# Kernel optimization log

Measured on AMD Instinct MI355X. Metric: run time of the kernel, lower is better.

## Reference

```python
import jax, jax.numpy as jnp
import numpy as np

BETA = 0.99  # EMA momentum from init_kwargs
EPS = 1e-12  # torch F.normalize eps


def _normalize(v):
    # matches torch.nn.functional.normalize (L2, dim=-1, eps clamp)
    n = jnp.maximum(jnp.linalg.norm(v, axis=-1, keepdims=True), EPS)
    return v / n


def setup_inputs() -> dict:
    key = jax.random.key(0)
    k1, k2 = jax.random.split(key)
    x = jax.random.normal(k1, (16384, 1024), dtype=jnp.float32)
    group_features = jax.random.uniform(k2, (8192, 1024), dtype=jnp.float32)
    return {"x": x, "group_features": group_features}


def reference(x, group_features):
    n_groups = group_features.shape[0]
    # assign_groups: cosine-sim argmax (normalized copies; does NOT modify x used below)
    xn = _normalize(x)
    gn = _normalize(group_features)
    logits = xn @ gn.T                      # [B, G]
    assignments = jnp.argmax(logits, axis=-1)  # [B] int

    # bincount over groups
    counts = jax.ops.segment_sum(
        jnp.ones_like(assignments, dtype=jnp.int32), assignments, num_segments=n_groups
    )  # [G]

    # scale only groups that received at least one sample by beta
    gf = jnp.where((counts > 0)[:, None], group_features * BETA, group_features)

    # scatter-add EMA contribution: (1-beta) * mean-style sum of raw x per group
    per_sample = x / counts[assignments][:, None].astype(x.dtype)  # safe: count>=1 for assigned
    contrib = jax.ops.segment_sum(per_sample, assignments, num_segments=n_groups)  # [G, D]
    gf = gf + (1.0 - BETA) * contrib

    return _normalize(gf)
```

## Files before the change

### kernel.cpp

```cpp
#include <hip/hip_runtime.h>

#define B_N 16384
#define G_N 8192
#define D_N 1024
#define NT 96

typedef unsigned short u16;
typedef unsigned long long u64;
typedef __attribute__((ext_vector_type(8))) short short8;
typedef __attribute__((ext_vector_type(16))) float f32x16;

#define AS1 __attribute__((address_space(1)))
#define AS3 __attribute__((address_space(3)))


__global__ __launch_bounds__(256) void k_norms(const float* __restrict__ g,
                                               float* __restrict__ invn) {
    const int j = blockIdx.x;
    const int t = threadIdx.x;
    const float4 v = *reinterpret_cast<const float4*>(&g[(size_t)j * D_N + t * 4]);
    float s = v.x * v.x + v.y * v.y + v.z * v.z + v.w * v.w;
#pragma unroll
    for (int off = 32; off >= 1; off >>= 1) s += __shfl_down(s, off, 64);
    __shared__ float wsum[4];
    if ((t & 63) == 0) wsum[t >> 6] = s;
    __syncthreads();
    if (t == 0) {
        const float tot = wsum[0] + wsum[1] + wsum[2] + wsum[3];
        invn[j] = 1.0f / fmaxf(sqrtf(tot), 1e-12f);
    }
}

__global__ void k_counts(const u64* __restrict__ pk, int* __restrict__ counts) {
    const int i = blockIdx.x * blockDim.x + threadIdx.x;
    if (i < B_N) {
        const int a = 8191 - (int)(pk[i] & 0x1FFFull);
        atomicAdd(&counts[a], 1);
    }
}

__global__ __launch_bounds__(256) void k_scatter(const float* __restrict__ x,
                                                 const u64* __restrict__ pk,
                                                 const int* __restrict__ counts,
                                                 float* __restrict__ contrib) {
    const int i = blockIdx.x;
    const int a = 8191 - (int)(pk[i] & 0x1FFFull);
    const float scale = 1.0f / (float)counts[a];
    const int t = threadIdx.x;
    const float4 v = *reinterpret_cast<const float4*>(&x[(size_t)i * D_N + t * 4]);
    float* dst = &contrib[(size_t)a * D_N + t * 4];
    atomicAdd(dst + 0, v.x * scale);
    atomicAdd(dst + 1, v.y * scale);
    atomicAdd(dst + 2, v.z * scale);
    atomicAdd(dst + 3, v.w * scale);
}

__global__ __launch_bounds__(256) void k_finalize(const float* __restrict__ g,
                                                  const int* __restrict__ counts,
                                                  float* __restrict__ out) {
    const int j = blockIdx.x;
    const int t = threadIdx.x;
    const float sc = (counts[j] > 0) ? 0.99f : 1.0f;
    const float4 gv = *reinterpret_cast<const float4*>(&g[(size_t)j * D_N + t * 4]);
    const float4 cv = *reinterpret_cast<const float4*>(&out[(size_t)j * D_N + t * 4]);
    float4 gf;
    gf.x = sc * gv.x + 0.01f * cv.x;
    gf.y = sc * gv.y + 0.01f * cv.y;
    gf.z = sc * gv.z + 0.01f * cv.z;
    gf.w = sc * gv.w + 0.01f * cv.w;
    float s = gf.x * gf.x + gf.y * gf.y + gf.z * gf.z + gf.w * gf.w;
#pragma unroll
    for (int off = 32; off >= 1; off >>= 1) s += __shfl_down(s, off, 64);
    __shared__ float wsum[4];
    __shared__ float s_inv;
    if ((t & 63) == 0) wsum[t >> 6] = s;
    __syncthreads();
    if (t == 0) s_inv = 1.0f / fmaxf(sqrtf(wsum[0] + wsum[1] + wsum[2] + wsum[3]), 1e-12f);
    __syncthreads();
    gf.x *= s_inv; gf.y *= s_inv; gf.z *= s_inv; gf.w *= s_inv;
    *reinterpret_cast<float4*>(&out[(size_t)j * D_N + t * 4]) = gf;
}


__device__ inline u16 f2bf_rtn(float f) {
    unsigned u = __float_as_uint(f);
    unsigned r = u + 0x7fffu + ((u >> 16) & 1u);
    return (u16)(r >> 16);
}
__device__ inline float bf2f(u16 h) { return __uint_as_float(((unsigned)h) << 16); }

__global__ __launch_bounds__(256) void k_split_pack(const float* __restrict__ src,
                                                    u16* __restrict__ hi,
                                                    u16* __restrict__ lo) {
    const int id = blockIdx.x * 256 + threadIdx.x;
    const int brick = id >> 7, c = id & 127;
    const int mu = brick >> 5, tau = brick & 31;
    const int ks = c >> 6, lane = c & 63;
    const int row = mu * 32 + (lane & 31);
    const int k = tau * 32 + ks * 16 + (lane >> 5) * 8;
    const float* s = src + (size_t)row * D_N + k;
    const float4 v0 = *reinterpret_cast<const float4*>(s);
    const float4 v1 = *reinterpret_cast<const float4*>(s + 4);
    const float f[8] = {v0.x, v0.y, v0.z, v0.w, v1.x, v1.y, v1.z, v1.w};
    short8 h, l;
#pragma unroll
    for (int j = 0; j < 8; ++j) {
        const u16 hj = f2bf_rtn(f[j]);
        h[j] = (short)hj;
        l[j] = (short)f2bf_rtn(f[j] - bf2f(hj));
    }
    *reinterpret_cast<short8*>(hi + (size_t)id * 8) = h;
    *reinterpret_cast<short8*>(lo + (size_t)id * 8) = l;
}


#define MFMA_BLK(S) do {                                                                   \
    __builtin_amdgcn_s_setprio(1);                                                         \
    _Pragma("unroll")                                                                      \
    for (int m = 0; m < 4; ++m)                                                            \
        _Pragma("unroll")                                                                  \
        for (int ks = 0; ks < 2; ++ks)                                                     \
            _Pragma("unroll")                                                              \
            for (int n = 0; n < 4; ++n)                                                    \
                acc[m][n] = __builtin_amdgcn_mfma_f32_32x32x16_bf16(                       \
                    afr[S][m][ks], bfr[S][n][ks], acc[m][n], 0, 0, 0);                     \
    __builtin_amdgcn_s_setprio(0);                                                         \
} while (0)

#define READS(BUF, S) do {                                                                 \
    const u16* aB = lds + (BUF) * 16384 + aRd;                                             \
    const u16* bB = lds + (BUF) * 16384 + 8192 + bRd;                                      \
    _Pragma("unroll")                                                                      \
    for (int n = 0; n < 4; ++n)                                                            \
        _Pragma("unroll")                                                                  \
        for (int ks = 0; ks < 2; ++ks)                                                     \
            bfr[S][n][ks] = *reinterpret_cast<const short8*>(bB + n * 1024 + ks * 512);    \
    _Pragma("unroll")                                                                      \
    for (int m = 0; m < 4; ++m)                                                            \
        _Pragma("unroll")                                                                  \
        for (int ks = 0; ks < 2; ++ks)                                                     \
            afr[S][m][ks] = *reinterpret_cast<const short8*>(aB + m * 1024 + ks * 512);    \
} while (0)

#define BODY(P, BRD, BSTG, SM, SR) do {                                                    \
    READS(BRD, SR);                                                                        \
    STG((P) + 3, BSTG);                                                                    \
    __builtin_amdgcn_sched_barrier(0);                                                     \
    MFMA_BLK(SM);                                                                          \
    asm volatile("s_waitcnt vmcnt(8)" ::: "memory");                                       \
    __builtin_amdgcn_s_barrier();                                                          \
} while (0)

__global__ __launch_bounds__(256, 1) void k_gemm_argmax(
    const u16* __restrict__ x_hi, const u16* __restrict__ x_lo,
    const u16* __restrict__ g_hi, const u16* __restrict__ g_lo,
    const float* __restrict__ invn, u64* __restrict__ pk) {

    __shared__ __align__(16) u16 lds[65536];

    const int bid = blockIdx.x;
    const int xcd = bid & 7, lcl = bid >> 3;
    const int mblk = xcd * 8 + ((lcl >> 3) & 7);
    const int nblk = (lcl & 7) + (lcl >> 6) * 8;
    const int mrow0 = mblk * 256, nrow0 = nblk * 256;

    const int tid = threadIdx.x;
    const int lane = tid & 63;
    const int w = tid >> 6;
    const int wr = w >> 1, wc = w & 1;
    const int l31 = lane & 31, l5 = lane >> 5;

    const int aRd = wr * 4096 + lane * 8;
    const int bRd = wc * 4096 + lane * 8;

    const int cOff = (tid & 127) * 8;
    const int hb = tid >> 7;
    const int wub = (tid & 192) * 8;
    const size_t aBase = ((size_t)(mblk * 8 + hb)) * 32768 + cOff;
    const size_t bBase = ((size_t)(nblk * 8 + hb)) * 32768 + cOff;

    auto STG = [&](int T, int buf) {
        const int Tc = T < NT ? T : NT - 1;
        const int term = Tc >> 5;
        const int tko = (Tc & 31) * 1024;
        const u16* xa = ((term == 1) ? x_lo : x_hi) + aBase + tko;
        const u16* gb = ((term == 2) ? g_lo : g_hi) + bBase + tko;
        u16* da = lds + buf * 16384 + wub;
        u16* db = da + 8192;
#pragma unroll
        for (int i = 0; i < 4; ++i)
            __builtin_amdgcn_global_load_lds((const AS1 void*)(xa + (size_t)i * 65536),
                                             (AS3 void*)(da + i * 2048), 16, 0, 0);
#pragma unroll
        for (int i = 0; i < 4; ++i)
            __builtin_amdgcn_global_load_lds((const AS1 void*)(gb + (size_t)i * 65536),
                                             (AS3 void*)(db + i * 2048), 16, 0, 0);
    };

    f32x16 acc[4][4];
#pragma unroll
    for (int m = 0; m < 4; ++m)
#pragma unroll
        for (int n = 0; n < 4; ++n)
#pragma unroll
            for (int r = 0; r < 16; ++r) acc[m][n][r] = 0.0f;

    short8 afr[2][4][2], bfr[2][4][2];

    STG(0, 0); STG(1, 1); STG(2, 2);
    asm volatile("s_waitcnt vmcnt(8)" ::: "memory");
    __builtin_amdgcn_s_barrier();
    READS(0, 0);

    for (int it = 0; it < 24; ++it) {
        const int p = it * 4;
        BODY(p,     1, 3, 0, 1);
        BODY(p + 1, 2, 0, 1, 0);
        BODY(p + 2, 3, 1, 0, 1);
        BODY(p + 3, 0, 2, 1, 0);
    }

    float inv[4];
#pragma unroll
    for (int n = 0; n < 4; ++n) inv[n] = invn[nrow0 + wc * 128 + n * 32 + l31];

#pragma unroll
    for (int m = 0; m < 4; ++m) {
#pragma unroll
        for (int r = 0; r < 16; ++r) {
            u64 p = 0;
#pragma unroll
            for (int n = 0; n < 4; ++n) {
                const float v = acc[m][n][r] * inv[n];
                unsigned u = __float_as_uint(v);
                u ^= (u >> 31) ? 0xFFFFFFFFu : 0x80000000u;
                const int col = nrow0 + wc * 128 + n * 32 + l31;
                const u64 cand = ((u64)u << 13) | (unsigned)(8191 - col);
                p = (cand > p) ? cand : p;
            }
#pragma unroll
            for (int msk = 1; msk < 32; msk <<= 1) {
                const u64 o = __shfl_xor(p, msk, 64);
                p = (o > p) ? o : p;
            }
            if (l31 == 0) {
                const int row = mrow0 + wr * 128 + m * 32 + (r & 3) + 8 * (r >> 2) + 4 * l5;
                atomicMax(&pk[row], p);
            }
        }
    }
}


__global__ __launch_bounds__(256) void k_argmax_fp32(const float* __restrict__ x,
                                                     const float* __restrict__ g,
                                                     const float* __restrict__ invn,
                                                     int* __restrict__ assign) {
    __shared__ __align__(16) float As[32][68];
    __shared__ __align__(16) float Bs[32][68];
    const int t = threadIdx.x;
    const int tx = t & 15;
    const int ty = t >> 4;
    const int row0 = blockIdx.x * 64;
    const int r_a = t >> 3;
    const int c4 = t & 7;
    float bestv[4]; int besti[4];
#pragma unroll
    for (int i = 0; i < 4; ++i) { bestv[i] = -3.0e38f; besti[i] = 0; }
    for (int jt = 0; jt < G_N / 64; ++jt) {
        float acc[4][4] = {};
        for (int kt = 0; kt < D_N / 32; ++kt) {
#pragma unroll
            for (int p = 0; p < 2; ++p) {
                const int r = r_a + p * 32;
                const float4 va = *reinterpret_cast<const float4*>(&x[(size_t)(row0 + r) * D_N + kt * 32 + c4 * 4]);
                As[c4 * 4 + 0][r] = va.x; As[c4 * 4 + 1][r] = va.y; As[c4 * 4 + 2][r] = va.z; As[c4 * 4 + 3][r] = va.w;
                const float4 vb = *reinterpret_cast<const float4*>(&g[(size_t)(jt * 64 + r) * D_N + kt * 32 + c4 * 4]);
                Bs[c4 * 4 + 0][r] = vb.x; Bs[c4 * 4 + 1][r] = vb.y; Bs[c4 * 4 + 2][r] = vb.z; Bs[c4 * 4 + 3][r] = vb.w;
            }
            __syncthreads();
#pragma unroll
            for (int k = 0; k < 32; ++k) {
                const float4 a = *reinterpret_cast<const float4*>(&As[k][ty * 4]);
                const float4 b = *reinterpret_cast<const float4*>(&Bs[k][tx * 4]);
                const float av[4] = {a.x, a.y, a.z, a.w};
                const float bv[4] = {b.x, b.y, b.z, b.w};
#pragma unroll
                for (int i = 0; i < 4; ++i)
#pragma unroll
                    for (int jj = 0; jj < 4; ++jj) acc[i][jj] += av[i] * bv[jj];
            }
            __syncthreads();
        }
#pragma unroll
        for (int jj = 0; jj < 4; ++jj) {
            const int col = jt * 64 + tx * 4 + jj;
            const float s = invn[col];
#pragma unroll
            for (int i = 0; i < 4; ++i) {
                const float v = acc[i][jj] * s;
                if (v > bestv[i]) { bestv[i] = v; besti[i] = col; }
            }
        }
    }
#pragma unroll
    for (int m = 1; m < 16; m <<= 1) {
#pragma unroll
        for (int i = 0; i < 4; ++i) {
            const float ov = __shfl_xor(bestv[i], m, 64);
            const int oi = __shfl_xor(besti[i], m, 64);
            if (ov > bestv[i] || (ov == bestv[i] && oi < besti[i])) { bestv[i] = ov; besti[i] = oi; }
        }
    }
    if (tx == 0) {
#pragma unroll
        for (int i = 0; i < 4; ++i) assign[row0 + ty * 4 + i] = besti[i];
    }
}

__global__ void k_counts_i(const int* __restrict__ assign, int* __restrict__ counts) {
    const int i = blockIdx.x * blockDim.x + threadIdx.x;
    if (i < B_N) atomicAdd(&counts[assign[i]], 1);
}

__global__ __launch_bounds__(256) void k_scatter_i(const float* __restrict__ x,
                                                   const int* __restrict__ assign,
                                                   const int* __restrict__ counts,
                                                   float* __restrict__ contrib) {
    const int i = blockIdx.x;
    const int a = assign[i];
    const float scale = 1.0f / (float)counts[a];
    const int t = threadIdx.x;
    const float4 v = *reinterpret_cast<const float4*>(&x[(size_t)i * D_N + t * 4]);
    float* dst = &contrib[(size_t)a * D_N + t * 4];
    atomicAdd(dst + 0, v.x * scale);
    atomicAdd(dst + 1, v.y * scale);
    atomicAdd(dst + 2, v.z * scale);
    atomicAdd(dst + 3, v.w * scale);
}


extern "C" void kernel_launch(void* const* d_in, const int* in_sizes, int n_in,
                              void* d_out, int out_size, void* d_ws, size_t ws_size,
                              hipStream_t stream) {
    const float* x = (const float*)d_in[0];
    const float* g = (const float*)d_in[1];
    float* out = (float*)d_out;

    char* ws = (char*)d_ws;
    u16*  x_hi  = (u16*)(ws);
    u16*  x_lo  = (u16*)(ws + 33554432);
    u16*  g_hi  = (u16*)(ws + 67108864);
    u16*  g_lo  = (u16*)(ws + 83886080);
    float* invn = (float*)(ws + 100663296);
    int* counts = (int*)(ws + 100696064);
    u64*   pk   = (u64*)(ws + 100728832);
    const size_t need = 100859904;

    hipMemsetAsync(out, 0, (size_t)G_N * D_N * sizeof(float), stream);

    if (ws_size >= need) {
        hipMemsetAsync(counts, 0, (size_t)G_N * sizeof(int), stream);
        hipMemsetAsync(pk, 0, (size_t)B_N * sizeof(u64), stream);
        k_norms<<<G_N, 256, 0, stream>>>(g, invn);
        k_split_pack<<<B_N * D_N / 8 / 256, 256, 0, stream>>>(x, x_hi, x_lo);
        k_split_pack<<<G_N * D_N / 8 / 256, 256, 0, stream>>>(g, g_hi, g_lo);
        k_gemm_argmax<<<2048, 256, 0, stream>>>(x_hi, x_lo, g_hi, g_lo, invn, pk);
        k_counts<<<B_N / 256, 256, 0, stream>>>(pk, counts);
        k_scatter<<<B_N, 256, 0, stream>>>(x, pk, counts, out);
        k_finalize<<<G_N, 256, 0, stream>>>(g, counts, out);
    } else {
        float* invn_f = (float*)ws;
        int* assign_f = (int*)(ws + (size_t)G_N * 4);
        int* counts_f = (int*)(ws + (size_t)(G_N + B_N) * 4);
        hipMemsetAsync(counts_f, 0, (size_t)G_N * sizeof(int), stream);
        k_norms<<<G_N, 256, 0, stream>>>(g, invn_f);
        k_argmax_fp32<<<B_N / 64, 256, 0, stream>>>(x, g, invn_f, assign_f);
        k_counts_i<<<B_N / 256, 256, 0, stream>>>(assign_f, counts_f);
        k_scatter_i<<<B_N, 256, 0, stream>>>(x, assign_f, counts_f, out);
        k_finalize<<<G_N, 256, 0, stream>>>(g, counts_f, out);
    }
}
```

Baseline: 1.063 ms.

## Load GEMM operand fragments directly from global memory, dropping the LDS pipeline

Removes the shared-memory staging pipeline (global_load_lds into four LDS buffers, barriers, LDS reads) and has each wave load its MFMA A/B fragments straight from global memory into registers, double-buffered across k-steps. The MFMA loop order is also changed so the k-slice is outermost. This is meant to eliminate LDS traffic and block-wide barriers. In exchange, there is no data sharing between waves, so each operand tile is fetched from global/L2 once per wave that uses it instead of once per block. Latency hiding now depends on a register prefetch only one step ahead.

```diff
diff --git a/kernel.cpp b/kernel.cpp
--- a/kernel.cpp
+++ b/kernel.cpp
@@ -9,9 +9,6 @@
 typedef unsigned long long u64;
 typedef __attribute__((ext_vector_type(8))) short short8;
 typedef __attribute__((ext_vector_type(16))) float f32x16;
-
-#define AS1 __attribute__((address_space(1)))
-#define AS3 __attribute__((address_space(3)))
 
 
 __global__ __launch_bounds__(256) void k_norms(const float* __restrict__ g,
@@ -117,9 +114,9 @@
 #define MFMA_BLK(S) do {                                                                   \
     __builtin_amdgcn_s_setprio(1);                                                         \
     _Pragma("unroll")                                                                      \
-    for (int m = 0; m < 4; ++m)                                                            \
+    for (int ks = 0; ks < 2; ++ks)                                                         \
         _Pragma("unroll")                                                                  \
-        for (int ks = 0; ks < 2; ++ks)                                                     \
+        for (int m = 0; m < 4; ++m)                                                        \
             _Pragma("unroll")                                                              \
             for (int n = 0; n < 4; ++n)                                                    \
                 acc[m][n] = __builtin_amdgcn_mfma_f32_32x32x16_bf16(                       \
@@ -127,36 +124,27 @@
     __builtin_amdgcn_s_setprio(0);                                                         \
 } while (0)
 
-#define READS(BUF, S) do {                                                                 \
-    const u16* aB = lds + (BUF) * 16384 + aRd;                                             \
-    const u16* bB = lds + (BUF) * 16384 + 8192 + bRd;                                      \
+#define LOADG(T, S) do {                                                                   \
+    const int Tc_ = (T) < NT ? (T) : NT - 1;                                               \
+    const u16* xa_ = ((Tc_ >> 5) == 1) ? x_lo : x_hi;                                      \
+    const u16* gb_ = ((Tc_ >> 5) == 2) ? g_lo : g_hi;                                      \
+    const size_t tk_ = (size_t)(Tc_ & 31) * 1024 + laneOff;                                \
+    _Pragma("unroll")                                                                      \
+    for (int m = 0; m < 4; ++m)                                                            \
+        _Pragma("unroll")                                                                  \
+        for (int ks = 0; ks < 2; ++ks)                                                     \
+            afr[S][m][ks] = *reinterpret_cast<const short8*>(xa_ + aBr[m] + tk_ + ks * 512);\
     _Pragma("unroll")                                                                      \
     for (int n = 0; n < 4; ++n)                                                            \
         _Pragma("unroll")                                                                  \
         for (int ks = 0; ks < 2; ++ks)                                                     \
-            bfr[S][n][ks] = *reinterpret_cast<const short8*>(bB + n * 1024 + ks * 512);    \
-    _Pragma("unroll")                                                                      \
-    for (int m = 0; m < 4; ++m)                                                            \
-        _Pragma("unroll")                                                                  \
-        for (int ks = 0; ks < 2; ++ks)                                                     \
-            afr[S][m][ks] = *reinterpret_cast<const short8*>(aB + m * 1024 + ks * 512);    \
-} while (0)
-
-#define BODY(P, BRD, BSTG, SM, SR) do {                                                    \
-    READS(BRD, SR);                                                                        \
-    STG((P) + 3, BSTG);                                                                    \
-    __builtin_amdgcn_sched_barrier(0);                                                     \
-    MFMA_BLK(SM);                                                                          \
-    asm volatile("s_waitcnt vmcnt(8)" ::: "memory");                                       \
-    __builtin_amdgcn_s_barrier();                                                          \
+            bfr[S][n][ks] = *reinterpret_cast<const short8*>(gb_ + bBr[n] + tk_ + ks * 512);\
 } while (0)
 
 __global__ __launch_bounds__(256, 1) void k_gemm_argmax(
     const u16* __restrict__ x_hi, const u16* __restrict__ x_lo,
     const u16* __restrict__ g_hi, const u16* __restrict__ g_lo,
     const float* __restrict__ invn, u64* __restrict__ pk) {
-
-    __shared__ __align__(16) u16 lds[65536];
 
     const int bid = blockIdx.x;
     const int xcd = bid & 7, lcl = bid >> 3;
@@ -170,32 +158,12 @@
     const int wr = w >> 1, wc = w & 1;
     const int l31 = lane & 31, l5 = lane >> 5;
 
-    const int aRd = wr * 4096 + lane * 8;
-    const int bRd = wc * 4096 + lane * 8;
-
-    const int cOff = (tid & 127) * 8;
-    const int hb = tid >> 7;
-    const int wub = (tid & 192) * 8;
-    const size_t aBase = ((size_t)(mblk * 8 + hb)) * 32768 + cOff;
-    const size_t bBase = ((size_t)(nblk * 8 + hb)) * 32768 + cOff;
-
-    auto STG = [&](int T, int buf) {
-        const int Tc = T < NT ? T : NT - 1;
-        const int term = Tc >> 5;
-        const int tko = (Tc & 31) * 1024;
-        const u16* xa = ((term == 1) ? x_lo : x_hi) + aBase + tko;
-        const u16* gb = ((term == 2) ? g_lo : g_hi) + bBase + tko;
-        u16* da = lds + buf * 16384 + wub;
-        u16* db = da + 8192;
-#pragma unroll
-        for (int i = 0; i < 4; ++i)
-            __builtin_amdgcn_global_load_lds((const AS1 void*)(xa + (size_t)i * 65536),
-                                             (AS3 void*)(da + i * 2048), 16, 0, 0);
-#pragma unroll
-        for (int i = 0; i < 4; ++i)
-            __builtin_amdgcn_global_load_lds((const AS1 void*)(gb + (size_t)i * 65536),
-                                             (AS3 void*)(db + i * 2048), 16, 0, 0);
-    };
+    const size_t laneOff = (size_t)lane * 8;
+    size_t aBr[4], bBr[4];
+#pragma unroll
+    for (int m = 0; m < 4; ++m) aBr[m] = (size_t)(mblk * 8 + wr * 4 + m) * 32768;
+#pragma unroll
+    for (int n = 0; n < 4; ++n) bBr[n] = (size_t)(nblk * 8 + wc * 4 + n) * 32768;
 
     f32x16 acc[4][4];
 #pragma unroll
@@ -207,17 +175,14 @@
 
     short8 afr[2][4][2], bfr[2][4][2];
 
-    STG(0, 0); STG(1, 1); STG(2, 2);
-    asm volatile("s_waitcnt vmcnt(8)" ::: "memory");
-    __builtin_amdgcn_s_barrier();
-    READS(0, 0);
-
-    for (int it = 0; it < 24; ++it) {
-        const int p = it * 4;
-        BODY(p,     1, 3, 0, 1);
-        BODY(p + 1, 2, 0, 1, 0);
-        BODY(p + 2, 3, 1, 0, 1);
-        BODY(p + 3, 0, 2, 1, 0);
+    LOADG(0, 0);
+
+    for (int it = 0; it < 48; ++it) {
+        const int q = it * 2;
+        LOADG(q + 1, 1);
+        MFMA_BLK(0);
+        LOADG(q + 2, 0);
+        MFMA_BLK(1);
     }
 
     float inv[4];
```

Result: faster. 987.3 us (-7.2%).
